# Kernel tuning notes

Hardware: AMD Instinct MI355X
Metric: run time of the kernel (lower is better)

## Reference

```python
import jax, jax.numpy as jnp
import numpy as np

N_NODES = 100000
N_EDGES = 1600000
IN_C, HID_C, OUT_C, N_CLS = 64, 128, 64, 20


def setup_inputs() -> dict:
    key = jax.random.key(0)
    ks = jax.random.split(key, 8)
    s = lambda k, sh: jax.random.normal(k, sh, dtype=jnp.float32) * (1.0 / np.sqrt(sh[0]))
    return {
        "x": jax.random.normal(ks[0], (N_NODES, IN_C), dtype=jnp.float32),
        "edge_index": jax.random.randint(ks[1], (2, N_EDGES), 0, N_NODES, dtype=jnp.int64),
        "w_self1": s(ks[2], (IN_C, HID_C)),
        "w_neigh1": s(ks[3], (IN_C, HID_C)),
        "b1": jnp.zeros((HID_C,), dtype=jnp.float32),
        "w_self2": s(ks[4], (HID_C, OUT_C)),
        "w_neigh2": s(ks[5], (HID_C, OUT_C)),
        "b2": jnp.zeros((OUT_C,), dtype=jnp.float32),
        "wc": s(ks[6], (OUT_C, N_CLS)),
        "bc": jnp.zeros((N_CLS,), dtype=jnp.float32),
    }


def _sage_mean(feat, src, dst, deg_inv, w_self, w_neigh, b):
    # gather messages along edges, segment-sum at destinations, mean-normalize
    msg_sum = jax.ops.segment_sum(feat[src], dst, num_segments=N_NODES)  # [N, d]
    h_neigh = msg_sum * deg_inv[:, None]
    return feat @ w_self + h_neigh @ w_neigh + b


def reference(x, edge_index, w_self1, w_neigh1, b1, w_self2, w_neigh2, b2, wc, bc):
    src, dst = edge_index[0], edge_index[1]
    deg = jax.ops.segment_sum(jnp.ones((src.shape[0],), dtype=x.dtype), dst,
                              num_segments=N_NODES)
    deg_inv = 1.0 / jnp.maximum(deg, 1.0)  # zero-degree nodes -> 0 neighbor mean
    h = jax.nn.relu(_sage_mean(x, src, dst, deg_inv, w_self1, w_neigh1, b1))
    h = jax.nn.relu(_sage_mean(h, src, dst, deg_inv, w_self2, w_neigh2, b2))
    return h @ wc + bc
```

## Files before the change

kernel.cpp:

```cpp
#include <hip/hip_runtime.h>

#define N_NODES 100000
#define N_EDGES 1600000
#define IN_C    64
#define HID_C   128
#define OUT_C   64
#define N_CLS   20

#define BUCKETS 196
#define XSL     8
#define WCAP    2560
#define EPB     4096
#define CAPB    44

#define CVT_BLOCKS 3125

typedef __attribute__((ext_vector_type(8))) short short8;
typedef __attribute__((ext_vector_type(4))) float floatx4;

__device__ __forceinline__ unsigned short f2bf(float f) {
    union { float f; unsigned u; } v; v.f = f;
    unsigned r = v.u + 0x7FFFu + ((v.u >> 16) & 1u);
    return (unsigned short)(r >> 16);
}
__device__ __forceinline__ unsigned pk2(float lo, float hi) {
    return (unsigned)f2bf(lo) | ((unsigned)f2bf(hi) << 16);
}
__device__ __forceinline__ float bflo(unsigned w) { return __uint_as_float(w << 16); }
__device__ __forceinline__ float bfhi(unsigned w) { return __uint_as_float(w & 0xFFFF0000u); }

__global__ __launch_bounds__(256) void prologue_kernel(
        const float* __restrict__ x,
        const float* __restrict__ ws1, const float* __restrict__ wn1,
        const float* __restrict__ ws2, const float* __restrict__ wn2,
        unsigned short* __restrict__ xb,
        unsigned short* __restrict__ wt1s, unsigned short* __restrict__ wt1n,
        unsigned short* __restrict__ wt2s, unsigned short* __restrict__ wt2n,
        int* __restrict__ bcnt)
{
    const int bid = blockIdx.x, tid = threadIdx.x;
    if (bid < CVT_BLOCKS) {
        int i = bid * 256 + tid;
        float4 a = ((const float4*)x)[(size_t)i * 2];
        float4 b = ((const float4*)x)[(size_t)i * 2 + 1];
        uint4 r;
        r.x = pk2(a.x, a.y); r.y = pk2(a.z, a.w);
        r.z = pk2(b.x, b.y); r.w = pk2(b.z, b.w);
        ((uint4*)xb)[i] = r;
    } else if (bid == CVT_BLOCKS) {
        for (int i = tid; i < BUCKETS * XSL; i += 256) bcnt[i] = 0;
    } else {
        int i = (bid - CVT_BLOCKS - 1) * 256 + tid;
        if (i < 8192) {
            int o = i >> 6, c = i & 63;
            wt1s[i] = f2bf(ws1[c * 128 + o]);
            wt1n[i] = f2bf(wn1[c * 128 + o]);
        } else if (i < 16384) {
            int j = i - 8192;
            int o = j >> 7, c = j & 127;
            wt2s[j] = f2bf(ws2[c * 64 + o]);
            wt2n[j] = f2bf(wn2[c * 64 + o]);
        }
    }
}

__global__ __launch_bounds__(256) void binA_kernel(
        const int* __restrict__ ei, int* __restrict__ bcnt,
        unsigned* __restrict__ bins)
{
    __shared__ unsigned lbins[BUCKETS * CAPB];
    __shared__ unsigned comp[EPB];
    __shared__ unsigned dsti[EPB];
    __shared__ int lcnt[BUCKETS], lofs[BUCKETS], gb[BUCKETS];
    __shared__ int sd[256];

    const int tid = threadIdx.x;
    const int xcd = blockIdx.x & (XSL - 1);
    const int e0  = blockIdx.x * EPB;

    for (int w = tid; w < BUCKETS; w += 256) lcnt[w] = 0;
    __syncthreads();

    for (int it = 0; it < EPB / 256; ++it) {
        int e = e0 + it * 256 + tid;
        if (e >= N_EDGES) break;
        int src = ei[e];
        int dst = ei[N_EDGES + e];
        int b = dst >> 9;
        unsigned pk = ((unsigned)(dst & 511) << 17) | (unsigned)src;
        int pos = atomicAdd(&lcnt[b], 1);
        if (pos < CAPB) {
            lbins[b * CAPB + pos] = pk;
        } else {
            int gp = atomicAdd(&bcnt[b * XSL + xcd], 1);
            if (gp < WCAP)
                bins[(unsigned)(b * XSL + xcd) * WCAP + gp] = pk;
        }
    }
    __syncthreads();

    int c = (tid < BUCKETS) ? min(lcnt[tid], CAPB) : 0;
    sd[tid] = c;
    __syncthreads();
    for (int off = 1; off < 256; off <<= 1) {
        int x = 0;
        if (tid >= off) x = sd[tid - off];
        __syncthreads();
        if (tid >= off) sd[tid] += x;
        __syncthreads();
    }
    if (tid < BUCKETS) lofs[tid] = sd[tid] - c;
    __syncthreads();
    const int T = sd[255];

    if (tid < BUCKETS) {
        int cw = min(lcnt[tid], CAPB);
        gb[tid] = (cw > 0) ? atomicAdd(&bcnt[tid * XSL + xcd], cw) : 0;
    }
    __syncthreads();

    if (tid < BUCKETS) {
        int cw = min(lcnt[tid], CAPB);
        int lo = lofs[tid];
        unsigned wb = (unsigned)(tid * XSL + xcd) * WCAP + (unsigned)gb[tid];
        for (int i = 0; i < cw; ++i) {
            comp[lo + i] = lbins[tid * CAPB + i];
            dsti[lo + i] = wb + i;
        }
    }
    __syncthreads();

    for (int i = tid; i < T; i += 256)
        bins[dsti[i]] = comp[i];
}

__global__ __launch_bounds__(256) void buildB_kernel(
        const int* __restrict__ bcnt, const unsigned* __restrict__ bins,
        int* __restrict__ row_ptr, int* __restrict__ sorted_src,
        float* __restrict__ dinv)
{
    __shared__ unsigned ent[16384];
    __shared__ int scnt[XSL], soff[XSL];
    __shared__ int cnt[512], lofs[512], cur[512];
    __shared__ int sd[256];
    __shared__ int gbase_s;

    const int b   = blockIdx.x;
    const int tid = threadIdx.x;
    const int node0 = b * 512;

    int part = 0;
    for (int w = tid; w < b * XSL; w += 256) part += min(bcnt[w], WCAP);
    sd[tid] = part;
    __syncthreads();
    for (int off = 128; off > 0; off >>= 1) {
        if (tid < off) sd[tid] += sd[tid + off];
        __syncthreads();
    }
    if (tid == 0) {
        gbase_s = sd[0];
        if (b == 0) row_ptr[N_NODES] = N_EDGES;
    }
    __syncthreads();

    if (tid < XSL) scnt[tid] = min(bcnt[b * XSL + tid], WCAP);
    { int i = tid; cnt[i] = 0; cnt[i + 256] = 0; }
    __syncthreads();
    if (tid == 0) {
        int acc = 0;
        for (int sl = 0; sl < XSL; ++sl) {
            soff[sl] = acc;
            acc += scnt[sl];
            if (acc > 16384) { scnt[sl] -= (acc - 16384); acc = 16384; }
        }
    }
    __syncthreads();

    for (int sl = 0; sl < XSL; ++sl) {
        int len = scnt[sl];
        const unsigned* seg = bins + (unsigned)(b * XSL + sl) * WCAP;
        int base = soff[sl];
        for (int i = tid; i < len; i += 256) {
            unsigned e = seg[i];
            ent[base + i] = e;
            atomicAdd((unsigned*)&cnt[e >> 17], 1u);
        }
    }
    __syncthreads();
    const int T = soff[XSL - 1] + scnt[XSL - 1];

    int a0 = cnt[2 * tid], a1 = cnt[2 * tid + 1];
    int s2 = a0 + a1;
    sd[tid] = s2;
    __syncthreads();
    for (int off = 1; off < 256; off <<= 1) {
        int x = 0;
        if (tid >= off) x = sd[tid - off];
        __syncthreads();
        if (tid >= off) sd[tid] += x;
        __syncthreads();
    }
    int excl = sd[tid] - s2;
    lofs[2 * tid]     = excl;
    lofs[2 * tid + 1] = excl + a0;
    cur[2 * tid]      = excl;
    cur[2 * tid + 1]  = excl + a0;
    __syncthreads();

    const int gbase = gbase_s;
    for (int j = tid; j < 512; j += 256) {
        int node = node0 + j;
        if (node < N_NODES) {
            row_ptr[node] = gbase + lofs[j];
            dinv[node] = 1.0f / (float)max(cnt[j], 1);
        }
    }
    for (int i = tid; i < T; i += 256) {
        unsigned e = ent[i];
        int dl = e >> 17;
        int p = atomicAdd((unsigned*)&cur[dl], 1u);
        sorted_src[gbase + p] = (int)(e & 0x1FFFFu);
    }
}

__global__ __launch_bounds__(256, 4) void fused1_kernel(
        const int* __restrict__ row_ptr, const int* __restrict__ srcs,
        const unsigned short* __restrict__ xb,
        const float* __restrict__ dinv,
        const unsigned short* __restrict__ wt1s,
        const unsigned short* __restrict__ wt1n,
        const float* __restrict__ b1,
        const unsigned short* __restrict__ wt2n,
        unsigned short* __restrict__ h1b,
        unsigned short* __restrict__ t2b)
{
    __shared__ unsigned short aggL[64 * 72];
    __shared__ unsigned short h1L[64 * 136];

    const int tid = threadIdx.x;
    const int node0 = blockIdx.x * 64;

    {
        const int q  = tid & 7;
        const int np = tid >> 3;
        const uint4* f4 = (const uint4*)xb;
        for (int half = 0; half < 2; ++half) {
            int lrow = half * 32 + np;
            int n = node0 + lrow;
            float a0=0,a1=0,a2=0,a3=0,a4=0,a5=0,a6=0,a7=0;
            if (n < N_NODES) {
                int beg = row_ptr[n];
                int end = row_ptr[n + 1];
                int e = beg;
                for (; e + 4 <= end; e += 4) {
                    int s0 = srcs[e], s1 = srcs[e+1], s2 = srcs[e+2], s3 = srcs[e+3];
                    uint4 v0 = f4[(size_t)s0 * 8 + q];
                    uint4 v1 = f4[(size_t)s1 * 8 + q];
                    uint4 v2 = f4[(size_t)s2 * 8 + q];
                    uint4 v3 = f4[(size_t)s3 * 8 + q];
                    a0 += bflo(v0.x); a1 += bfhi(v0.x); a2 += bflo(v0.y); a3 += bfhi(v0.y);
                    a4 += bflo(v0.z); a5 += bfhi(v0.z); a6 += bflo(v0.w); a7 += bfhi(v0.w);
                    a0 += bflo(v1.x); a1 += bfhi(v1.x); a2 += bflo(v1.y); a3 += bfhi(v1.y);
                    a4 += bflo(v1.z); a5 += bfhi(v1.z); a6 += bflo(v1.w); a7 += bfhi(v1.w);
                    a0 += bflo(v2.x); a1 += bfhi(v2.x); a2 += bflo(v2.y); a3 += bfhi(v2.y);
                    a4 += bflo(v2.z); a5 += bfhi(v2.z); a6 += bflo(v2.w); a7 += bfhi(v2.w);
                    a0 += bflo(v3.x); a1 += bfhi(v3.x); a2 += bflo(v3.y); a3 += bfhi(v3.y);
                    a4 += bflo(v3.z); a5 += bfhi(v3.z); a6 += bflo(v3.w); a7 += bfhi(v3.w);
                }
                for (; e < end; ++e) {
                    uint4 v = f4[(size_t)srcs[e] * 8 + q];
                    a0 += bflo(v.x); a1 += bfhi(v.x); a2 += bflo(v.y); a3 += bfhi(v.y);
                    a4 += bflo(v.z); a5 += bfhi(v.z); a6 += bflo(v.w); a7 += bfhi(v.w);
                }
                float di = dinv[n];
                a0*=di; a1*=di; a2*=di; a3*=di; a4*=di; a5*=di; a6*=di; a7*=di;
            }
            uint4 r;
            r.x = pk2(a0, a1); r.y = pk2(a2, a3);
            r.z = pk2(a4, a5); r.w = pk2(a6, a7);
            *(uint4*)(aggL + lrow * 72 + q * 8) = r;
        }
    }
    __syncthreads();

    const int lane = tid & 63;
    const int wv   = tid >> 6;
    const int quad = lane >> 4;
    const int col  = lane & 15;
    const int nrow = wv * 16 + col;
    const int nl = node0 + nrow;
    const int nc = min(nl, N_NODES - 1);
    const bool ok = nl < N_NODES;

    {
        const short8 bs0 = *(const short8*)(xb + (size_t)nc * 64 +      quad * 8);
        const short8 bs1 = *(const short8*)(xb + (size_t)nc * 64 + 32 + quad * 8);
        const short8 bn0 = *(const short8*)(aggL + nrow * 72 +      quad * 8);
        const short8 bn1 = *(const short8*)(aggL + nrow * 72 + 32 + quad * 8);

#pragma unroll
        for (int mt = 0; mt < 8; ++mt) {
            int m = mt * 16 + col;
            const short8 as0 = *(const short8*)(wt1s + (size_t)m * 64 +      quad * 8);
            const short8 as1 = *(const short8*)(wt1s + (size_t)m * 64 + 32 + quad * 8);
            const short8 an0 = *(const short8*)(wt1n + (size_t)m * 64 +      quad * 8);
            const short8 an1 = *(const short8*)(wt1n + (size_t)m * 64 + 32 + quad * 8);
            floatx4 acc = {0.f, 0.f, 0.f, 0.f};
            acc = __builtin_amdgcn_mfma_f32_16x16x32_bf16(as0, bs0, acc, 0, 0, 0);
            acc = __builtin_amdgcn_mfma_f32_16x16x32_bf16(as1, bs1, acc, 0, 0, 0);
            acc = __builtin_amdgcn_mfma_f32_16x16x32_bf16(an0, bn0, acc, 0, 0, 0);
            acc = __builtin_amdgcn_mfma_f32_16x16x32_bf16(an1, bn1, acc, 0, 0, 0);
            int och = mt * 16 + quad * 4;
            float4 bv = *(const float4*)(b1 + och);
            ushort4 r;
            r.x = f2bf(fmaxf(acc[0] + bv.x, 0.f));
            r.y = f2bf(fmaxf(acc[1] + bv.y, 0.f));
            r.z = f2bf(fmaxf(acc[2] + bv.z, 0.f));
            r.w = f2bf(fmaxf(acc[3] + bv.w, 0.f));
            *(ushort4*)(h1L + nrow * 136 + och) = r;
            if (ok) *(ushort4*)(h1b + (size_t)nl * 128 + och) = r;
        }
    }
    __syncthreads();

    {
        short8 bfr[4];
#pragma unroll
        for (int kc = 0; kc < 4; ++kc)
            bfr[kc] = *(const short8*)(h1L + nrow * 136 + kc * 32 + quad * 8);

#pragma unroll
        for (int mt = 0; mt < 4; ++mt) {
            int m = mt * 16 + col;
            floatx4 acc = {0.f, 0.f, 0.f, 0.f};
#pragma unroll
            for (int kc = 0; kc < 4; ++kc) {
                const short8 a = *(const short8*)(wt2n + (size_t)m * 128 + kc * 32 + quad * 8);
                acc = __builtin_amdgcn_mfma_f32_16x16x32_bf16(a, bfr[kc], acc, 0, 0, 0);
            }
            if (ok) {
                int och = mt * 16 + quad * 4;
                ushort4 r;
                r.x = f2bf(acc[0]); r.y = f2bf(acc[1]);
                r.z = f2bf(acc[2]); r.w = f2bf(acc[3]);
                *(ushort4*)(t2b + (size_t)nl * 64 + och) = r;
            }
        }
    }
}

__global__ __launch_bounds__(256, 4) void fused2_kernel(
        const int* __restrict__ row_ptr, const int* __restrict__ srcs,
        const unsigned short* __restrict__ t2b,
        const float* __restrict__ dinv,
        const unsigned short* __restrict__ h1b,
        const unsigned short* __restrict__ wt2s,
        const float* __restrict__ b2,
        const float* __restrict__ wc,
        const float* __restrict__ bc,
        float* __restrict__ out)
{
    __shared__ float aggL[64 * 68];
    __shared__ float hs[64][65];
    __shared__ float wcs[64 * N_CLS];
    __shared__ float bcs[N_CLS];

    const int tid = threadIdx.x;
    const int node0 = blockIdx.x * 64;

    for (int t = tid; t < 64 * N_CLS; t += 256) wcs[t] = wc[t];
    if (tid < N_CLS) bcs[tid] = bc[tid];

    {
        const int q  = tid & 7;
        const int np = tid >> 3;
        const uint4* f4 = (const uint4*)t2b;
        for (int half = 0; half < 2; ++half) {
            int lrow = half * 32 + np;
            int n = node0 + lrow;
            float a0=0,a1=0,a2=0,a3=0,a4=0,a5=0,a6=0,a7=0;
            if (n < N_NODES) {
                int beg = row_ptr[n];
                int end = row_ptr[n + 1];
                int e = beg;
                for (; e + 4 <= end; e += 4) {
                    int s0 = srcs[e], s1 = srcs[e+1], s2 = srcs[e+2], s3 = srcs[e+3];
                    uint4 v0 = f4[(size_t)s0 * 8 + q];
                    uint4 v1 = f4[(size_t)s1 * 8 + q];
                    uint4 v2 = f4[(size_t)s2 * 8 + q];
                    uint4 v3 = f4[(size_t)s3 * 8 + q];
                    a0 += bflo(v0.x); a1 += bfhi(v0.x); a2 += bflo(v0.y); a3 += bfhi(v0.y);
                    a4 += bflo(v0.z); a5 += bfhi(v0.z); a6 += bflo(v0.w); a7 += bfhi(v0.w);
                    a0 += bflo(v1.x); a1 += bfhi(v1.x); a2 += bflo(v1.y); a3 += bfhi(v1.y);
                    a4 += bflo(v1.z); a5 += bfhi(v1.z); a6 += bflo(v1.w); a7 += bfhi(v1.w);
                    a0 += bflo(v2.x); a1 += bfhi(v2.x); a2 += bflo(v2.y); a3 += bfhi(v2.y);
                    a4 += bflo(v2.z); a5 += bfhi(v2.z); a6 += bflo(v2.w); a7 += bfhi(v2.w);
                    a0 += bflo(v3.x); a1 += bfhi(v3.x); a2 += bflo(v3.y); a3 += bfhi(v3.y);
                    a4 += bflo(v3.z); a5 += bfhi(v3.z); a6 += bflo(v3.w); a7 += bfhi(v3.w);
                }
                for (; e < end; ++e) {
                    uint4 v = f4[(size_t)srcs[e] * 8 + q];
                    a0 += bflo(v.x); a1 += bfhi(v.x); a2 += bflo(v.y); a3 += bfhi(v.y);
                    a4 += bflo(v.z); a5 += bfhi(v.z); a6 += bflo(v.w); a7 += bfhi(v.w);
                }
                float di = dinv[n];
                a0*=di; a1*=di; a2*=di; a3*=di; a4*=di; a5*=di; a6*=di; a7*=di;
            }
            float* d = aggL + lrow * 68 + q * 8;
            *(float4*)(d)     = make_float4(a0, a1, a2, a3);
            *(float4*)(d + 4) = make_float4(a4, a5, a6, a7);
        }
    }
    __syncthreads();

    const int lane = tid & 63;
    const int wv   = tid >> 6;
    const int quad = lane >> 4;
    const int col  = lane & 15;
    const int nrow = wv * 16 + col;
    const int nl = node0 + nrow;
    const int nc = min(nl, N_NODES - 1);

    {
        short8 b[4];
#pragma unroll
        for (int kc = 0; kc < 4; ++kc)
            b[kc] = *(const short8*)(h1b + (size_t)nc * 128 + kc * 32 + quad * 8);

#pragma unroll
        for (int mt = 0; mt < 4; ++mt) {
            int m = mt * 16 + col;
            floatx4 acc = {0.f, 0.f, 0.f, 0.f};
#pragma unroll
            for (int kc = 0; kc < 4; ++kc) {
                const short8 a = *(const short8*)(wt2s + (size_t)m * 128 + kc * 32 + quad * 8);
                acc = __builtin_amdgcn_mfma_f32_16x16x32_bf16(a, b[kc], acc, 0, 0, 0);
            }
            int och = mt * 16 + quad * 4;
            float4 av = *(const float4*)(aggL + nrow * 68 + och);
            float4 bv = *(const float4*)(b2 + och);
            hs[nrow][och + 0] = fmaxf(acc[0] + av.x + bv.x, 0.f);
            hs[nrow][och + 1] = fmaxf(acc[1] + av.y + bv.y, 0.f);
            hs[nrow][och + 2] = fmaxf(acc[2] + av.z + bv.z, 0.f);
            hs[nrow][och + 3] = fmaxf(acc[3] + av.w + bv.w, 0.f);
        }
    }
    __syncthreads();

    for (int o = tid; o < 64 * N_CLS; o += 256) {
        int n = o / N_CLS, cls = o % N_CLS;
        if (node0 + n >= N_NODES) continue;
        float s = bcs[cls];
#pragma unroll
        for (int k = 0; k < 64; ++k) s += hs[n][k] * wcs[k * N_CLS + cls];
        out[(size_t)(node0 + n) * N_CLS + cls] = s;
    }
}


extern "C" void kernel_launch(void* const* d_in, const int* in_sizes, int n_in,
                              void* d_out, int out_size, void* d_ws, size_t ws_size,
                              hipStream_t stream)
{
    const float* x        = (const float*)d_in[0];
    const int*   ei       = (const int*)  d_in[1];
    const float* w_self1  = (const float*)d_in[2];
    const float* w_neigh1 = (const float*)d_in[3];
    const float* b1       = (const float*)d_in[4];
    const float* w_self2  = (const float*)d_in[5];
    const float* w_neigh2 = (const float*)d_in[6];
    const float* b2       = (const float*)d_in[7];
    const float* wc       = (const float*)d_in[8];
    const float* bc       = (const float*)d_in[9];
    float* out = (float*)d_out;

    const size_t N = N_NODES;
    int*      bcnt    = (int*)d_ws;
    int*      row_ptr = bcnt + BUCKETS * XSL + 8;
    unsigned* bins    = (unsigned*)(row_ptr + N + 8);
    int*      s_src   = (int*)(bins + BUCKETS * XSL * WCAP);
    float*    dinv    = (float*)(s_src + N_EDGES);
    unsigned short* xb    = (unsigned short*)(dinv + N);
    unsigned short* h1b   = xb + 64 * N;
    unsigned short* t2b   = h1b + 128 * N;
    unsigned short* wt1s  = t2b + 64 * N;
    unsigned short* wt1n  = wt1s + 8192;
    unsigned short* wt2s  = wt1n + 8192;
    unsigned short* wt2n  = wt2s + 8192;

    const int PB  = CVT_BLOCKS + 1 + 64;
    const int EB2 = (N_EDGES + EPB - 1) / EPB;
    const int MB  = (N_NODES + 63) / 64;

    prologue_kernel<<<PB, 256, 0, stream>>>(x, w_self1, w_neigh1, w_self2,
                                            w_neigh2, xb, wt1s, wt1n, wt2s,
                                            wt2n, bcnt);
    binA_kernel<<<EB2, 256, 0, stream>>>(ei, bcnt, bins);
    buildB_kernel<<<BUCKETS, 256, 0, stream>>>(bcnt, bins, row_ptr, s_src, dinv);
    fused1_kernel<<<MB, 256, 0, stream>>>(row_ptr, s_src, xb, dinv,
                                          wt1s, wt1n, b1, wt2n, h1b, t2b);
    fused2_kernel<<<MB, 256, 0, stream>>>(row_ptr, s_src, t2b, dinv,
                                          h1b, wt2s, b2, wc, bc, out);
}
```

Measured before the change: 301.3 us.

## Move layer-2 self GEMM into fused1, drop h1 round-trip, unroll gathers by 8

The layer-2 self-projection (h1 @ w_self2 + b2) now runs in fused1 while h1 is still in shared memory and is stored as a 64-wide bf16 tensor s2b. This replaces writing the 128-wide h1 to global memory and reading it back in fused2. fused2 becomes a gather plus an elementwise combine followed by the classifier, with no MFMA stage and less shared memory. fused1 reuses one shared buffer for both stages behind an extra barrier. Both kernels unroll the neighbour gather by 8 and raise the occupancy hint to 6 blocks per SM, which adds register pressure and rounds the self term to bf16 before the add.

```diff
diff --git a/kernel.cpp b/kernel.cpp
--- a/kernel.cpp
+++ b/kernel.cpp
@@ -28,6 +28,10 @@
 }
 __device__ __forceinline__ float bflo(unsigned w) { return __uint_as_float(w << 16); }
 __device__ __forceinline__ float bfhi(unsigned w) { return __uint_as_float(w & 0xFFFF0000u); }
+
+#define ACC8(v) do { \
+    a0 += bflo((v).x); a1 += bfhi((v).x); a2 += bflo((v).y); a3 += bfhi((v).y); \
+    a4 += bflo((v).z); a5 += bfhi((v).z); a6 += bflo((v).w); a7 += bfhi((v).w); } while (0)
 
 __global__ __launch_bounds__(256) void prologue_kernel(
         const float* __restrict__ x,
@@ -223,7 +227,7 @@
     }
 }
 
-__global__ __launch_bounds__(256, 4) void fused1_kernel(
+__global__ __launch_bounds__(256, 6) void fused1_kernel(
         const int* __restrict__ row_ptr, const int* __restrict__ srcs,
         const unsigned short* __restrict__ xb,
         const float* __restrict__ dinv,
@@ -231,11 +235,12 @@
         const unsigned short* __restrict__ wt1n,
         const float* __restrict__ b1,
         const unsigned short* __restrict__ wt2n,
-        unsigned short* __restrict__ h1b,
-        unsigned short* __restrict__ t2b)
-{
-    __shared__ unsigned short aggL[64 * 72];
-    __shared__ unsigned short h1L[64 * 136];
+        const unsigned short* __restrict__ wt2s,
+        const float* __restrict__ b2,
+        unsigned short* __restrict__ t2b,
+        unsigned short* __restrict__ s2b)
+{
+    __shared__ unsigned short sbuf[64 * 136];
 
     const int tid = threadIdx.x;
     const int node0 = blockIdx.x * 64;
@@ -252,25 +257,23 @@
                 int beg = row_ptr[n];
                 int end = row_ptr[n + 1];
                 int e = beg;
-                for (; e + 4 <= end; e += 4) {
-                    int s0 = srcs[e], s1 = srcs[e+1], s2 = srcs[e+2], s3 = srcs[e+3];
+                for (; e + 8 <= end; e += 8) {
+                    int s0 = srcs[e],   s1 = srcs[e+1], s2 = srcs[e+2], s3 = srcs[e+3];
+                    int s4 = srcs[e+4], s5 = srcs[e+5], s6 = srcs[e+6], s7 = srcs[e+7];
                     uint4 v0 = f4[(size_t)s0 * 8 + q];
                     uint4 v1 = f4[(size_t)s1 * 8 + q];
                     uint4 v2 = f4[(size_t)s2 * 8 + q];
                     uint4 v3 = f4[(size_t)s3 * 8 + q];
-                    a0 += bflo(v0.x); a1 += bfhi(v0.x); a2 += bflo(v0.y); a3 += bfhi(v0.y);
-                    a4 += bflo(v0.z); a5 += bfhi(v0.z); a6 += bflo(v0.w); a7 += bfhi(v0.w);
-                    a0 += bflo(v1.x); a1 += bfhi(v1.x); a2 += bflo(v1.y); a3 += bfhi(v1.y);
-                    a4 += bflo(v1.z); a5 += bfhi(v1.z); a6 += bflo(v1.w); a7 += bfhi(v1.w);
-                    a0 += bflo(v2.x); a1 += bfhi(v2.x); a2 += bflo(v2.y); a3 += bfhi(v2.y);
-                    a4 += bflo(v2.z); a5 += bfhi(v2.z); a6 += bflo(v2.w); a7 += bfhi(v2.w);
-                    a0 += bflo(v3.x); a1 += bfhi(v3.x); a2 += bflo(v3.y); a3 += bfhi(v3.y);
-                    a4 += bflo(v3.z); a5 += bfhi(v3.z); a6 += bflo(v3.w); a7 += bfhi(v3.w);
+                    uint4 v4 = f4[(size_t)s4 * 8 + q];
+                    uint4 v5 = f4[(size_t)s5 * 8 + q];
+                    uint4 v6 = f4[(size_t)s6 * 8 + q];
+                    uint4 v7 = f4[(size_t)s7 * 8 + q];
+                    ACC8(v0); ACC8(v1); ACC8(v2); ACC8(v3);
+                    ACC8(v4); ACC8(v5); ACC8(v6); ACC8(v7);
                 }
                 for (; e < end; ++e) {
                     uint4 v = f4[(size_t)srcs[e] * 8 + q];
-                    a0 += bflo(v.x); a1 += bfhi(v.x); a2 += bflo(v.y); a3 += bfhi(v.y);
-                    a4 += bflo(v.z); a5 += bfhi(v.z); a6 += bflo(v.w); a7 += bfhi(v.w);
+                    ACC8(v);
                 }
                 float di = dinv[n];
                 a0*=di; a1*=di; a2*=di; a3*=di; a4*=di; a5*=di; a6*=di; a7*=di;
@@ -278,7 +281,7 @@
             uint4 r;
             r.x = pk2(a0, a1); r.y = pk2(a2, a3);
             r.z = pk2(a4, a5); r.w = pk2(a6, a7);
-            *(uint4*)(aggL + lrow * 72 + q * 8) = r;
+            *(uint4*)(sbuf + lrow * 72 + q * 8) = r;
         }
     }
     __syncthreads();
@@ -295,8 +298,9 @@
     {
         const short8 bs0 = *(const short8*)(xb + (size_t)nc * 64 +      quad * 8);
         const short8 bs1 = *(const short8*)(xb + (size_t)nc * 64 + 32 + quad * 8);
-        const short8 bn0 = *(const short8*)(aggL + nrow * 72 +      quad * 8);
-        const short8 bn1 = *(const short8*)(aggL + nrow * 72 + 32 + quad * 8);
+        const short8 bn0 = *(const short8*)(sbuf + nrow * 72 +      quad * 8);
+        const short8 bn1 = *(const short8*)(sbuf + nrow * 72 + 32 + quad * 8);
+        __syncthreads();
 
 #pragma unroll
         for (int mt = 0; mt < 8; ++mt) {
@@ -317,8 +321,7 @@
             r.y = f2bf(fmaxf(acc[1] + bv.y, 0.f));
             r.z = f2bf(fmaxf(acc[2] + bv.z, 0.f));
             r.w = f2bf(fmaxf(acc[3] + bv.w, 0.f));
-            *(ushort4*)(h1L + nrow * 136 + och) = r;
-            if (ok) *(ushort4*)(h1b + (size_t)nl * 128 + och) = r;
+            *(ushort4*)(sbuf + nrow * 136 + och) = r;
         }
     }
     __syncthreads();
@@ -327,41 +330,46 @@
         short8 bfr[4];
 #pragma unroll
         for (int kc = 0; kc < 4; ++kc)
-            bfr[kc] = *(const short8*)(h1L + nrow * 136 + kc * 32 + quad * 8);
+            bfr[kc] = *(const short8*)(sbuf + nrow * 136 + kc * 32 + quad * 8);
 
 #pragma unroll
         for (int mt = 0; mt < 4; ++mt) {
             int m = mt * 16 + col;
-            floatx4 acc = {0.f, 0.f, 0.f, 0.f};
+            floatx4 at = {0.f, 0.f, 0.f, 0.f};
+            floatx4 as = {0.f, 0.f, 0.f, 0.f};
 #pragma unroll
             for (int kc = 0; kc < 4; ++kc) {
-                const short8 a = *(const short8*)(wt2n + (size_t)m * 128 + kc * 32 + quad * 8);
-                acc = __builtin_amdgcn_mfma_f32_16x16x32_bf16(a, bfr[kc], acc, 0, 0, 0);
+                const short8 an = *(const short8*)(wt2n + (size_t)m * 128 + kc * 32 + quad * 8);
+                const short8 aw = *(const short8*)(wt2s + (size_t)m * 128 + kc * 32 + quad * 8);
+                at = __builtin_amdgcn_mfma_f32_16x16x32_bf16(an, bfr[kc], at, 0, 0, 0);
+                as = __builtin_amdgcn_mfma_f32_16x16x32_bf16(aw, bfr[kc], as, 0, 0, 0);
             }
             if (ok) {
                 int och = mt * 16 + quad * 4;
-                ushort4 r;
-                r.x = f2bf(acc[0]); r.y = f2bf(acc[1]);
-                r.z = f2bf(acc[2]); r.w = f2bf(acc[3]);
-                *(ushort4*)(t2b + (size_t)nl * 64 + och) = r;
+                ushort4 rt;
+                rt.x = f2bf(at[0]); rt.y = f2bf(at[1]);
+                rt.z = f2bf(at[2]); rt.w = f2bf(at[3]);
+                *(ushort4*)(t2b + (size_t)nl * 64 + och) = rt;
+                float4 bv = *(const float4*)(b2 + och);
+                ushort4 rs;
+                rs.x = f2bf(as[0] + bv.x); rs.y = f2bf(as[1] + bv.y);
+                rs.z = f2bf(as[2] + bv.z); rs.w = f2bf(as[3] + bv.w);
+                *(ushort4*)(s2b + (size_t)nl * 64 + och) = rs;
             }
         }
     }
 }
 
-__global__ __launch_bounds__(256, 4) void fused2_kernel(
+__global__ __launch_bounds__(256, 6) void fused2_kernel(
         const int* __restrict__ row_ptr, const int* __restrict__ srcs,
         const unsigned short* __restrict__ t2b,
+        const unsigned short* __restrict__ s2b,
         const float* __restrict__ dinv,
-        const unsigned short* __restrict__ h1b,
-        const unsigned short* __restrict__ wt2s,
-        const float* __restrict__ b2,
         const float* __restrict__ wc,
         const float* __restrict__ bc,
         float* __restrict__ out)
 {
-    __shared__ float aggL[64 * 68];
-    __shared__ float hs[64][65];
+    __shared__ float hs[64][68];
     __shared__ float wcs[64 * N_CLS];
     __shared__ float bcs[N_CLS];
 
@@ -378,71 +386,41 @@
         for (int half = 0; half < 2; ++half) {
             int lrow = half * 32 + np;
             int n = node0 + lrow;
-            float a0=0,a1=0,a2=0,a3=0,a4=0,a5=0,a6=0,a7=0;
             if (n < N_NODES) {
+                float a0=0,a1=0,a2=0,a3=0,a4=0,a5=0,a6=0,a7=0;
                 int beg = row_ptr[n];
                 int end = row_ptr[n + 1];
                 int e = beg;
-                for (; e + 4 <= end; e += 4) {
-                    int s0 = srcs[e], s1 = srcs[e+1], s2 = srcs[e+2], s3 = srcs[e+3];
+                for (; e + 8 <= end; e += 8) {
+                    int s0 = srcs[e],   s1 = srcs[e+1], s2 = srcs[e+2], s3 = srcs[e+3];
+                    int s4 = srcs[e+4], s5 = srcs[e+5], s6 = srcs[e+6], s7 = srcs[e+7];
                     uint4 v0 = f4[(size_t)s0 * 8 + q];
                     uint4 v1 = f4[(size_t)s1 * 8 + q];
                     uint4 v2 = f4[(size_t)s2 * 8 + q];
                     uint4 v3 = f4[(size_t)s3 * 8 + q];
-                    a0 += bflo(v0.x); a1 += bfhi(v0.x); a2 += bflo(v0.y); a3 += bfhi(v0.y);
-                    a4 += bflo(v0.z); a5 += bfhi(v0.z); a6 += bflo(v0.w); a7 += bfhi(v0.w);
-                    a0 += bflo(v1.x); a1 += bfhi(v1.x); a2 += bflo(v1.y); a3 += bfhi(v1.y);
-                    a4 += bflo(v1.z); a5 += bfhi(v1.z); a6 += bflo(v1.w); a7 += bfhi(v1.w);
-                    a0 += bflo(v2.x); a1 += bfhi(v2.x); a2 += bflo(v2.y); a3 += bfhi(v2.y);
-                    a4 += bflo(v2.z); a5 += bfhi(v2.z); a6 += bflo(v2.w); a7 += bfhi(v2.w);
-                    a0 += bflo(v3.x); a1 += bfhi(v3.x); a2 += bflo(v3.y); a3 += bfhi(v3.y);
-                    a4 += bflo(v3.z); a5 += bfhi(v3.z); a6 += bflo(v3.w); a7 += bfhi(v3.w);
+                    uint4 v4 = f4[(size_t)s4 * 8 + q];
+                    uint4 v5 = f4[(size_t)s5 * 8 + q];
+                    uint4 v6 = f4[(size_t)s6 * 8 + q];
+                    uint4 v7 = f4[(size_t)s7 * 8 + q];
+                    ACC8(v0); ACC8(v1); ACC8(v2); ACC8(v3);
+                    ACC8(v4); ACC8(v5); ACC8(v6); ACC8(v7);
                 }
                 for (; e < end; ++e) {
                     uint4 v = f4[(size_t)srcs[e] * 8 + q];
-                    a0 += bflo(v.x); a1 += bfhi(v.x); a2 += bflo(v.y); a3 += bfhi(v.y);
-                    a4 += bflo(v.z); a5 += bfhi(v.z); a6 += bflo(v.w); a7 += bfhi(v.w);
+                    ACC8(v);
                 }
                 float di = dinv[n];
-                a0*=di; a1*=di; a2*=di; a3*=di; a4*=di; a5*=di; a6*=di; a7*=di;
+                uint4 sv = *(const uint4*)(s2b + (size_t)n * 64 + q * 8);
+                float* d = hs[lrow] + q * 8;
+                d[0] = fmaxf(a0 * di + bflo(sv.x), 0.f);
+                d[1] = fmaxf(a1 * di + bfhi(sv.x), 0.f);
+                d[2] = fmaxf(a2 * di + bflo(sv.y), 0.f);
+                d[3] = fmaxf(a3 * di + bfhi(sv.y), 0.f);
+                d[4] = fmaxf(a4 * di + bflo(sv.z), 0.f);
+                d[5] = fmaxf(a5 * di + bfhi(sv.z), 0.f);
+                d[6] = fmaxf(a6 * di + bflo(sv.w), 0.f);
+                d[7] = fmaxf(a7 * di + bfhi(sv.w), 0.f);
             }
-            float* d = aggL + lrow * 68 + q * 8;
-            *(float4*)(d)     = make_float4(a0, a1, a2, a3);
-            *(float4*)(d + 4) = make_float4(a4, a5, a6, a7);
-        }
-    }
-    __syncthreads();
-
-    const int lane = tid & 63;
-    const int wv   = tid >> 6;
-    const int quad = lane >> 4;
-    const int col  = lane & 15;
-    const int nrow = wv * 16 + col;
-    const int nl = node0 + nrow;
-    const int nc = min(nl, N_NODES - 1);
-
-    {
-        short8 b[4];
-#pragma unroll
-        for (int kc = 0; kc < 4; ++kc)
-            b[kc] = *(const short8*)(h1b + (size_t)nc * 128 + kc * 32 + quad * 8);
-
-#pragma unroll
-        for (int mt = 0; mt < 4; ++mt) {
-            int m = mt * 16 + col;
-            floatx4 acc = {0.f, 0.f, 0.f, 0.f};
-#pragma unroll
-            for (int kc = 0; kc < 4; ++kc) {
-                const short8 a = *(const short8*)(wt2s + (size_t)m * 128 + kc * 32 + quad * 8);
-                acc = __builtin_amdgcn_mfma_f32_16x16x32_bf16(a, b[kc], acc, 0, 0, 0);
-            }
-            int och = mt * 16 + quad * 4;
-            float4 av = *(const float4*)(aggL + nrow * 68 + och);
-            float4 bv = *(const float4*)(b2 + och);
-            hs[nrow][och + 0] = fmaxf(acc[0] + av.x + bv.x, 0.f);
-            hs[nrow][och + 1] = fmaxf(acc[1] + av.y + bv.y, 0.f);
-            hs[nrow][och + 2] = fmaxf(acc[2] + av.z + bv.z, 0.f);
-            hs[nrow][och + 3] = fmaxf(acc[3] + av.w + bv.w, 0.f);
         }
     }
     __syncthreads();
@@ -481,9 +459,9 @@
     int*      s_src   = (int*)(bins + BUCKETS * XSL * WCAP);
     float*    dinv    = (float*)(s_src + N_EDGES);
     unsigned short* xb    = (unsigned short*)(dinv + N);
-    unsigned short* h1b   = xb + 64 * N;
-    unsigned short* t2b   = h1b + 128 * N;
-    unsigned short* wt1s  = t2b + 64 * N;
+    unsigned short* t2b   = xb + 64 * N;
+    unsigned short* s2b   = t2b + 64 * N;
+    unsigned short* wt1s  = s2b + 64 * N;
     unsigned short* wt1n  = wt1s + 8192;
     unsigned short* wt2s  = wt1n + 8192;
     unsigned short* wt2n  = wt2s + 8192;
@@ -498,7 +476,8 @@
     binA_kernel<<<EB2, 256, 0, stream>>>(ei, bcnt, bins);
     buildB_kernel<<<BUCKETS, 256, 0, stream>>>(bcnt, bins, row_ptr, s_src, dinv);
     fused1_kernel<<<MB, 256, 0, stream>>>(row_ptr, s_src, xb, dinv,
-                                          wt1s, wt1n, b1, wt2n, h1b, t2b);
-    fused2_kernel<<<MB, 256, 0, stream>>>(row_ptr, s_src, t2b, dinv,
-                                          h1b, wt2s, b2, wc, bc, out);
-}
+                                          wt1s, wt1n, b1, wt2n, wt2s, b2,
+                                          t2b, s2b);
+    fused2_kernel<<<MB, 256, 0, stream>>>(row_ptr, s_src, t2b, s2b, dinv,
+                                          wc, bc, out);
+}
```

After: 313.6 us. 1.04x slower.
